# Kernel tuning notes

Measured on AMD Instinct MI355X. Metric: run time of the kernel, lower is better.

## Reference

```python
import jax, jax.numpy as jnp
import numpy as np


def setup_inputs() -> dict:
    key = jax.random.key(0)
    k1, k2, k3 = jax.random.split(key, 3)
    B, M, N, D = 8, 12, 32, 256
    C = N * N          # Conv2d channel dim == N*N (see permute/view in source)
    R = 2              # reduction
    x = jax.random.normal(k1, (B, M, N, D), dtype=jnp.float32)
    W1 = jax.random.normal(k2, (C // R, C), dtype=jnp.float32) * 0.02  # Conv2d(C, C//R, 1, bias=False)
    W2 = jax.random.normal(k3, (C, C // R), dtype=jnp.float32) * 0.02  # Conv2d(C//R, C, 1, bias=False)
    return {"x": x, "W1": W1, "W2": W2}


def _mycorr(x):
    # Pearson correlation across feature dim D -> [B, M, N, N] adjacency
    xm = x - x.mean(axis=-1, keepdims=True)
    cov = jnp.einsum('bmnd,bmkd->bmnk', xm, xm)
    diag = jnp.diagonal(cov, axis1=-2, axis2=-1)                 # [B, M, N]
    norm = jnp.sqrt(jnp.clip(diag, 1e-12))
    return cov / (norm[..., :, None] * norm[..., None, :])


def reference(x, W1, W2):
    B, M, N, D = x.shape
    adj = _mycorr(x)

    # Fused pairwise-combo + mean over concat dim (2D):
    #   cat([Wh_i, pos_ij * Wh_j], -1).mean(-1) = (sum_d Wh_i + sum_d pos_ij*Wh_j) / (2D)
    # pos_ij[d] = 1 where Wh_i[d] == Wh_j[d] else 2   (source's where(diff==0, 1, 2))
    Wi = x[:, :, :, None, :]          # [B, M, N, 1, D]
    Wj = x[:, :, None, :, :]          # [B, M, 1, N, D]
    pos = jnp.where(Wi == Wj, jnp.float32(1.0), jnp.float32(2.0))
    e0 = (x.sum(-1)[:, :, :, None] + (pos * Wj).sum(-1)) / (2.0 * D)  # [B, M, N, N]

    # squeeze-excite style 1x1-conv MLP over the N*N channel dim
    ef = e0.reshape(B, M, N * N).transpose(0, 2, 1)                   # [B, C=N*N, M]
    h = jax.nn.relu(jnp.einsum('oc,bcm->bom', W1, ef))                # [B, C//R, M]
    e2 = jnp.einsum('co,bom->bcm', W2, h)                             # [B, C, M]
    e = jax.nn.sigmoid(e2.transpose(0, 2, 1).reshape(B, M, N, N))

    att = jnp.where(adj > 0, e, jnp.float32(-1e12))
    att = jax.nn.softmax(att, axis=-1)
    return jnp.einsum('bmnk,bmkd->bmnd', att, x)
```

## Files before the change

### kernel.cpp

```cpp
#include <hip/hip_runtime.h>


__device__ __forceinline__ float sum4(float4 v){ return v.x+v.y+v.z+v.w; }
__device__ __forceinline__ float dot4(float4 a, float4 b){
    return a.x*b.x + a.y*b.y + a.z*b.z + a.w*b.w;
}
__device__ __forceinline__ void fma4s(float4& a, float s, float4 v){
    a.x += s*v.x; a.y += s*v.y; a.z += s*v.z; a.w += s*v.w;
}

__global__ __launch_bounds__(256) void k1(const float* __restrict__ x,
                                          const float* __restrict__ W1,
                                          float* __restrict__ A1t,
                                          float* __restrict__ Sg,
                                          float* __restrict__ covg) {
    int bid = blockIdx.x;
    if (bid < 128) {
        __shared__ float Rl[4][32];
        __shared__ float Cl[4][32];
        int w = threadIdx.x >> 6, l = threadIdx.x & 63;
        int o = bid*4 + w;
        const float4* W14 = (const float4*)(W1 + o*1024);
        float4 v0 = W14[l], v1 = W14[l+64], v2 = W14[l+128], v3 = W14[l+192];
        float r0 = sum4(v0), r1 = sum4(v1), r2 = sum4(v2), r3 = sum4(v3);
        #pragma unroll
        for (int m = 1; m < 8; m <<= 1) {
            r0 += __shfl_xor(r0, m, 8);
            r1 += __shfl_xor(r1, m, 8);
            r2 += __shfl_xor(r2, m, 8);
            r3 += __shfl_xor(r3, m, 8);
        }
        float4 cp;
        cp.x = v0.x+v1.x+v2.x+v3.x; cp.y = v0.y+v1.y+v2.y+v3.y;
        cp.z = v0.z+v1.z+v2.z+v3.z; cp.w = v0.w+v1.w+v2.w+v3.w;
        #pragma unroll
        for (int m = 8; m < 64; m <<= 1) {
            cp.x += __shfl_xor(cp.x, m);
            cp.y += __shfl_xor(cp.y, m);
            cp.z += __shfl_xor(cp.z, m);
            cp.w += __shfl_xor(cp.w, m);
        }
        if ((l & 7) == 0) {
            int nb = l >> 3;
            Rl[w][nb]    = r0; Rl[w][nb+8]  = r1;
            Rl[w][nb+16] = r2; Rl[w][nb+24] = r3;
        }
        if (l < 8) *((float4*)&Cl[w][l*4]) = cp;
        __syncthreads();
        if (l < 32) {
            float a = (Rl[w][l] + 2.f*Cl[w][l] - W1[o*1024 + 33*l]) * (1.f/512.f);
            A1t[l*512 + o] = a;
        }
    } else {
        int bm = bid - 128;
        int t = threadIdx.x;
        __shared__ float4 xs4[32][65];
        __shared__ float Gp[8][32][36];
        __shared__ alignas(16) float S_l[32];
        const float4* x4 = (const float4*)x;
        #pragma unroll
        for (int i = 0; i < 8; ++i) {
            int idx = t + 256*i;
            xs4[idx >> 6][idx & 63] = x4[bm*2048 + idx];
        }
        __syncthreads();
        {
            int n = t >> 3, dq = t & 7;
            float s = 0.f;
            #pragma unroll
            for (int j = 0; j < 8; ++j) s += sum4(xs4[n][dq + 8*j]);
            s += __shfl_xor(s, 1, 8);
            s += __shfl_xor(s, 2, 8);
            s += __shfl_xor(s, 4, 8);
            if (dq == 0) { S_l[n] = s; Sg[bm*32 + n] = s; }
        }
        {
            int qs = t >> 5, tid = t & 31, rt = tid >> 2, ct = tid & 3;
            float g[4][8];
            #pragma unroll
            for (int i = 0; i < 4; ++i)
                #pragma unroll
                for (int j = 0; j < 8; ++j) g[i][j] = 0.f;
            #pragma unroll
            for (int qq = 0; qq < 8; ++qq) {
                int q = qs*8 + qq;
                float4 a0 = xs4[rt][q],    a1 = xs4[rt+8][q];
                float4 a2 = xs4[rt+16][q], a3 = xs4[rt+24][q];
                #pragma unroll
                for (int j = 0; j < 8; ++j) {
                    float4 b = xs4[ct + 4*j][q];
                    g[0][j] += dot4(a0, b); g[1][j] += dot4(a1, b);
                    g[2][j] += dot4(a2, b); g[3][j] += dot4(a3, b);
                }
            }
            #pragma unroll
            for (int i = 0; i < 4; ++i)
                #pragma unroll
                for (int j = 0; j < 8; ++j)
                    Gp[qs][rt + 8*i][ct + 4*j] = g[i][j];
        }
        __syncthreads();
        {
            int n = t >> 3, k0 = (t & 7)*4;
            float4 g = {0.f,0.f,0.f,0.f};
            #pragma unroll
            for (int qs = 0; qs < 8; ++qs) {
                float4 p = *((const float4*)&Gp[qs][n][k0]);
                g.x += p.x; g.y += p.y; g.z += p.z; g.w += p.w;
            }
            float sn = S_l[n] * (1.f/256.f);
            float4 sk = *((const float4*)&S_l[k0]);
            float4 cv;
            cv.x = g.x - sn*sk.x; cv.y = g.y - sn*sk.y;
            cv.z = g.z - sn*sk.z; cv.w = g.w - sn*sk.w;
            ((float4*)covg)[bm*256 + t] = cv;
        }
    }
}

__global__ __launch_bounds__(256) void k2(const float* __restrict__ W2,
                                          const float* __restrict__ A1t,
                                          const float* __restrict__ Sg,
                                          float* __restrict__ Et) {
    __shared__ alignas(16) float S_l[8][32];
    __shared__ float hl[8][516];
    int t = threadIdx.x;
    int cT = blockIdx.x, bmG = blockIdx.y;
    {
        int bl = t >> 5, n = t & 31;
        S_l[bl][n] = Sg[(bmG*8 + bl)*32 + n];
    }
    __syncthreads();
    {
        const float4* A4 = (const float4*)A1t;
        #pragma unroll
        for (int part = 0; part < 4; ++part) {
            int o4 = part*256 + t;
            int bl = o4 >> 7, ol = o4 & 127;
            float4 hacc = {0.f,0.f,0.f,0.f};
            #pragma unroll 8
            for (int n = 0; n < 32; ++n)
                fma4s(hacc, S_l[bl][n], A4[n*128 + ol]);
            hacc.x = fmaxf(hacc.x, 0.f); hacc.y = fmaxf(hacc.y, 0.f);
            hacc.z = fmaxf(hacc.z, 0.f); hacc.w = fmaxf(hacc.w, 0.f);
            *((float4*)&hl[bl][ol*4]) = hacc;
        }
    }
    __syncthreads();
    {
        int olane = t & 15, cg = t >> 4;
        const float4* W24 = (const float4*)W2;
        #pragma unroll
        for (int ci = 0; ci < 4; ++ci) {
            int c = cT*64 + cg*4 + ci;
            float acc[8] = {0.f,0.f,0.f,0.f,0.f,0.f,0.f,0.f};
            #pragma unroll
            for (int oo = 0; oo < 8; ++oo) {
                float4 w = W24[c*128 + oo*16 + olane];
                #pragma unroll
                for (int bl = 0; bl < 8; ++bl)
                    acc[bl] += dot4(w, *((const float4*)&hl[bl][(oo*16+olane)*4]));
            }
            #pragma unroll
            for (int bl = 0; bl < 8; ++bl) {
                float a = acc[bl];
                a += __shfl_xor(a, 1, 16);
                a += __shfl_xor(a, 2, 16);
                a += __shfl_xor(a, 4, 16);
                a += __shfl_xor(a, 8, 16);
                if (olane == 0)
                    Et[(bmG*8 + bl)*1024 + c] = 1.f / (1.f + __expf(-a));
            }
        }
    }
}

__global__ __launch_bounds__(256) void k4(const float* __restrict__ x,
                                          const float* __restrict__ covg,
                                          const float* __restrict__ Et,
                                          float* __restrict__ out) {
    int bm = blockIdx.x >> 1;
    int h  = blockIdx.x & 1;
    int t  = threadIdx.x;
    __shared__ float4 xs4[32][33];
    __shared__ float att_l[32][36];
    const float4* x4 = (const float4*)x;
    #pragma unroll
    for (int i = 0; i < 4; ++i) {
        int idx = t + 256*i;
        int n = idx >> 5, dq = idx & 31;
        xs4[n][dq] = x4[bm*2048 + n*64 + h*32 + dq];
    }
    {
        float4 cv = ((const float4*)covg)[bm*256 + t];
        float4 e  = ((const float4*)Et)[bm*256 + t];
        float4 lg;
        lg.x = cv.x > 0.f ? e.x : -1e12f;
        lg.y = cv.y > 0.f ? e.y : -1e12f;
        lg.z = cv.z > 0.f ? e.z : -1e12f;
        lg.w = cv.w > 0.f ? e.w : -1e12f;
        float m = fmaxf(fmaxf(lg.x, lg.y), fmaxf(lg.z, lg.w));
        m = fmaxf(m, __shfl_xor(m, 1, 8));
        m = fmaxf(m, __shfl_xor(m, 2, 8));
        m = fmaxf(m, __shfl_xor(m, 4, 8));
        float4 p;
        p.x = __expf(lg.x - m); p.y = __expf(lg.y - m);
        p.z = __expf(lg.z - m); p.w = __expf(lg.w - m);
        float s = p.x + p.y + p.z + p.w;
        s += __shfl_xor(s, 1, 8);
        s += __shfl_xor(s, 2, 8);
        s += __shfl_xor(s, 4, 8);
        float inv = 1.f / s;
        p.x *= inv; p.y *= inv; p.z *= inv; p.w *= inv;
        *((float4*)&att_l[t >> 3][(t & 7)*4]) = p;
    }
    __syncthreads();
    {
        int txl = t & 31, wy = t >> 5;
        int r0 = wy*4;
        float4 acc0={0,0,0,0}, acc1={0,0,0,0}, acc2={0,0,0,0}, acc3={0,0,0,0};
        #pragma unroll
        for (int kq = 0; kq < 8; ++kq) {
            float4 xa = xs4[kq*4+0][txl];
            float4 xb = xs4[kq*4+1][txl];
            float4 xc = xs4[kq*4+2][txl];
            float4 xd = xs4[kq*4+3][txl];
            float4 w0 = *((const float4*)&att_l[r0+0][kq*4]);
            float4 w1 = *((const float4*)&att_l[r0+1][kq*4]);
            float4 w2 = *((const float4*)&att_l[r0+2][kq*4]);
            float4 w3 = *((const float4*)&att_l[r0+3][kq*4]);
            fma4s(acc0,w0.x,xa); fma4s(acc0,w0.y,xb); fma4s(acc0,w0.z,xc); fma4s(acc0,w0.w,xd);
            fma4s(acc1,w1.x,xa); fma4s(acc1,w1.y,xb); fma4s(acc1,w1.z,xc); fma4s(acc1,w1.w,xd);
            fma4s(acc2,w2.x,xa); fma4s(acc2,w2.y,xb); fma4s(acc2,w2.z,xc); fma4s(acc2,w2.w,xd);
            fma4s(acc3,w3.x,xa); fma4s(acc3,w3.y,xb); fma4s(acc3,w3.z,xc); fma4s(acc3,w3.w,xd);
        }
        float4* out4 = (float4*)out;
        out4[bm*2048 + (r0+0)*64 + h*32 + txl] = acc0;
        out4[bm*2048 + (r0+1)*64 + h*32 + txl] = acc1;
        out4[bm*2048 + (r0+2)*64 + h*32 + txl] = acc2;
        out4[bm*2048 + (r0+3)*64 + h*32 + txl] = acc3;
    }
}

extern "C" void kernel_launch(void* const* d_in, const int* in_sizes, int n_in,
                              void* d_out, int out_size, void* d_ws, size_t ws_size,
                              hipStream_t stream) {
    const float* x  = (const float*)d_in[0];
    const float* W1 = (const float*)d_in[1];
    const float* W2 = (const float*)d_in[2];
    float* out = (float*)d_out;
    float* ws  = (float*)d_ws;

    float* A1t  = ws;
    float* Sg   = ws + 16384;
    float* covg = ws + 19456;
    float* Et   = ws + 117760;

    k1<<<224, 256, 0, stream>>>(x, W1, A1t, Sg, covg);
    k2<<<dim3(16, 12), 256, 0, stream>>>(W2, A1t, Sg, Et);
    k4<<<192, 256, 0, stream>>>(x, covg, Et, out);
}
```

Measured before the change: 86.91 us.

## Fuse covariance, SE MLP and softmax-aggregate into one per-(b,m) kernel

Splits out the W1 precompute into its own small kernel. The covariance, hidden-layer MLP, W2 projection with sigmoid, masked softmax and attention aggregation now run in one kernel with one block per (b,m), using shared memory only. This removes two launches and the global round trips for the covariance, row sums and gate values. In exchange, each of the 96 blocks re-reads all of W2 with no batching across (b,m), so W2 traffic rises. Only 96 blocks run, which leaves many compute units idle.

```diff
diff --git a/kernel.cpp b/kernel.cpp
--- a/kernel.cpp
+++ b/kernel.cpp
@@ -9,191 +9,156 @@
     a.x += s*v.x; a.y += s*v.y; a.z += s*v.z; a.w += s*v.w;
 }
 
-__global__ __launch_bounds__(256) void k1(const float* __restrict__ x,
-                                          const float* __restrict__ W1,
-                                          float* __restrict__ A1t,
-                                          float* __restrict__ Sg,
-                                          float* __restrict__ covg) {
-    int bid = blockIdx.x;
-    if (bid < 128) {
-        __shared__ float Rl[4][32];
-        __shared__ float Cl[4][32];
-        int w = threadIdx.x >> 6, l = threadIdx.x & 63;
-        int o = bid*4 + w;
-        const float4* W14 = (const float4*)(W1 + o*1024);
-        float4 v0 = W14[l], v1 = W14[l+64], v2 = W14[l+128], v3 = W14[l+192];
-        float r0 = sum4(v0), r1 = sum4(v1), r2 = sum4(v2), r3 = sum4(v3);
-        #pragma unroll
-        for (int m = 1; m < 8; m <<= 1) {
-            r0 += __shfl_xor(r0, m, 8);
-            r1 += __shfl_xor(r1, m, 8);
-            r2 += __shfl_xor(r2, m, 8);
-            r3 += __shfl_xor(r3, m, 8);
-        }
-        float4 cp;
-        cp.x = v0.x+v1.x+v2.x+v3.x; cp.y = v0.y+v1.y+v2.y+v3.y;
-        cp.z = v0.z+v1.z+v2.z+v3.z; cp.w = v0.w+v1.w+v2.w+v3.w;
-        #pragma unroll
-        for (int m = 8; m < 64; m <<= 1) {
-            cp.x += __shfl_xor(cp.x, m);
-            cp.y += __shfl_xor(cp.y, m);
-            cp.z += __shfl_xor(cp.z, m);
-            cp.w += __shfl_xor(cp.w, m);
-        }
-        if ((l & 7) == 0) {
-            int nb = l >> 3;
-            Rl[w][nb]    = r0; Rl[w][nb+8]  = r1;
-            Rl[w][nb+16] = r2; Rl[w][nb+24] = r3;
-        }
-        if (l < 8) *((float4*)&Cl[w][l*4]) = cp;
-        __syncthreads();
-        if (l < 32) {
-            float a = (Rl[w][l] + 2.f*Cl[w][l] - W1[o*1024 + 33*l]) * (1.f/512.f);
-            A1t[l*512 + o] = a;
-        }
-    } else {
-        int bm = bid - 128;
-        int t = threadIdx.x;
-        __shared__ float4 xs4[32][65];
-        __shared__ float Gp[8][32][36];
-        __shared__ alignas(16) float S_l[32];
-        const float4* x4 = (const float4*)x;
-        #pragma unroll
-        for (int i = 0; i < 8; ++i) {
-            int idx = t + 256*i;
-            xs4[idx >> 6][idx & 63] = x4[bm*2048 + idx];
-        }
-        __syncthreads();
-        {
-            int n = t >> 3, dq = t & 7;
-            float s = 0.f;
-            #pragma unroll
-            for (int j = 0; j < 8; ++j) s += sum4(xs4[n][dq + 8*j]);
-            s += __shfl_xor(s, 1, 8);
-            s += __shfl_xor(s, 2, 8);
-            s += __shfl_xor(s, 4, 8);
-            if (dq == 0) { S_l[n] = s; Sg[bm*32 + n] = s; }
-        }
-        {
-            int qs = t >> 5, tid = t & 31, rt = tid >> 2, ct = tid & 3;
-            float g[4][8];
-            #pragma unroll
-            for (int i = 0; i < 4; ++i)
-                #pragma unroll
-                for (int j = 0; j < 8; ++j) g[i][j] = 0.f;
-            #pragma unroll
-            for (int qq = 0; qq < 8; ++qq) {
-                int q = qs*8 + qq;
-                float4 a0 = xs4[rt][q],    a1 = xs4[rt+8][q];
-                float4 a2 = xs4[rt+16][q], a3 = xs4[rt+24][q];
-                #pragma unroll
-                for (int j = 0; j < 8; ++j) {
-                    float4 b = xs4[ct + 4*j][q];
-                    g[0][j] += dot4(a0, b); g[1][j] += dot4(a1, b);
-                    g[2][j] += dot4(a2, b); g[3][j] += dot4(a3, b);
-                }
+__global__ __launch_bounds__(256) void kA(const float* __restrict__ W1,
+                                          float* __restrict__ A1t) {
+    __shared__ float Rl[4][32];
+    __shared__ float Cl[4][32];
+    int w = threadIdx.x >> 6, l = threadIdx.x & 63;
+    int o = blockIdx.x*4 + w;
+    const float4* W14 = (const float4*)(W1 + o*1024);
+    float4 v0 = W14[l], v1 = W14[l+64], v2 = W14[l+128], v3 = W14[l+192];
+    float r0 = sum4(v0), r1 = sum4(v1), r2 = sum4(v2), r3 = sum4(v3);
+    #pragma unroll
+    for (int m = 1; m < 8; m <<= 1) {
+        r0 += __shfl_xor(r0, m, 8);
+        r1 += __shfl_xor(r1, m, 8);
+        r2 += __shfl_xor(r2, m, 8);
+        r3 += __shfl_xor(r3, m, 8);
+    }
+    float4 cp;
+    cp.x = v0.x+v1.x+v2.x+v3.x; cp.y = v0.y+v1.y+v2.y+v3.y;
+    cp.z = v0.z+v1.z+v2.z+v3.z; cp.w = v0.w+v1.w+v2.w+v3.w;
+    #pragma unroll
+    for (int m = 8; m < 64; m <<= 1) {
+        cp.x += __shfl_xor(cp.x, m);
+        cp.y += __shfl_xor(cp.y, m);
+        cp.z += __shfl_xor(cp.z, m);
+        cp.w += __shfl_xor(cp.w, m);
+    }
+    if ((l & 7) == 0) {
+        int nb = l >> 3;
+        Rl[w][nb]    = r0; Rl[w][nb+8]  = r1;
+        Rl[w][nb+16] = r2; Rl[w][nb+24] = r3;
+    }
+    if (l < 8) *((float4*)&Cl[w][l*4]) = cp;
+    __syncthreads();
+    if (l < 32) {
+        float a = (Rl[w][l] + 2.f*Cl[w][l] - W1[o*1024 + 33*l]) * (1.f/512.f);
+        A1t[l*512 + o] = a;
+    }
+}
+
+__global__ __launch_bounds__(256) void kM(const float* __restrict__ x,
+                                          const float* __restrict__ A1t,
+                                          const float* __restrict__ W2,
+                                          float* __restrict__ out) {
+    int bm = blockIdx.x;
+    int t  = threadIdx.x;
+    __shared__ float4 xs4[32][65];
+    __shared__ float Gp[4][32][37];
+    __shared__ alignas(16) float S_l[32];
+    __shared__ alignas(16) float hl[520];
+    __shared__ alignas(16) float el[1024];
+    __shared__ alignas(16) float att_l[32][36];
+
+    const float4* x4 = (const float4*)x;
+    #pragma unroll
+    for (int i = 0; i < 8; ++i) {
+        int idx = t + 256*i;
+        xs4[idx >> 6][idx & 63] = x4[bm*2048 + idx];
+    }
+    __syncthreads();
+
+    {
+        int n = t >> 3, dq = t & 7;
+        float s = 0.f;
+        #pragma unroll
+        for (int j = 0; j < 8; ++j) s += sum4(xs4[n][dq + 8*j]);
+        s += __shfl_xor(s, 1, 8);
+        s += __shfl_xor(s, 2, 8);
+        s += __shfl_xor(s, 4, 8);
+        if (dq == 0) S_l[n] = s;
+    }
+    {
+        int w = t >> 6, l = t & 63, rt = l >> 3, ct = l & 7;
+        float g[4][4];
+        #pragma unroll
+        for (int i = 0; i < 4; ++i)
+            #pragma unroll
+            for (int j = 0; j < 4; ++j) g[i][j] = 0.f;
+        #pragma unroll 4
+        for (int qq = 0; qq < 16; ++qq) {
+            int q = w*16 + qq;
+            float4 a0 = xs4[rt][q],    a1 = xs4[rt+8][q];
+            float4 a2 = xs4[rt+16][q], a3 = xs4[rt+24][q];
+            #pragma unroll
+            for (int j = 0; j < 4; ++j) {
+                float4 b = xs4[ct + 8*j][q];
+                g[0][j] += dot4(a0, b); g[1][j] += dot4(a1, b);
+                g[2][j] += dot4(a2, b); g[3][j] += dot4(a3, b);
             }
-            #pragma unroll
-            for (int i = 0; i < 4; ++i)
-                #pragma unroll
-                for (int j = 0; j < 8; ++j)
-                    Gp[qs][rt + 8*i][ct + 4*j] = g[i][j];
-        }
-        __syncthreads();
-        {
-            int n = t >> 3, k0 = (t & 7)*4;
-            float4 g = {0.f,0.f,0.f,0.f};
-            #pragma unroll
-            for (int qs = 0; qs < 8; ++qs) {
-                float4 p = *((const float4*)&Gp[qs][n][k0]);
-                g.x += p.x; g.y += p.y; g.z += p.z; g.w += p.w;
-            }
-            float sn = S_l[n] * (1.f/256.f);
-            float4 sk = *((const float4*)&S_l[k0]);
-            float4 cv;
-            cv.x = g.x - sn*sk.x; cv.y = g.y - sn*sk.y;
-            cv.z = g.z - sn*sk.z; cv.w = g.w - sn*sk.w;
-            ((float4*)covg)[bm*256 + t] = cv;
-        }
-    }
-}
-
-__global__ __launch_bounds__(256) void k2(const float* __restrict__ W2,
-                                          const float* __restrict__ A1t,
-                                          const float* __restrict__ Sg,
-                                          float* __restrict__ Et) {
-    __shared__ alignas(16) float S_l[8][32];
-    __shared__ float hl[8][516];
-    int t = threadIdx.x;
-    int cT = blockIdx.x, bmG = blockIdx.y;
-    {
-        int bl = t >> 5, n = t & 31;
-        S_l[bl][n] = Sg[(bmG*8 + bl)*32 + n];
-    }
-    __syncthreads();
-    {
+        }
+        #pragma unroll
+        for (int i = 0; i < 4; ++i)
+            #pragma unroll
+            for (int j = 0; j < 4; ++j)
+                Gp[w][rt + 8*i][ct + 8*j] = g[i][j];
+    }
+    __syncthreads();
+
+    {
+        int n = t >> 3, k0 = (t & 7)*4;
+        float sn = S_l[n] * (1.f/256.f);
+        float4 cv;
+        #pragma unroll
+        for (int c = 0; c < 4; ++c) {
+            float g = Gp[0][n][k0+c] + Gp[1][n][k0+c]
+                    + Gp[2][n][k0+c] + Gp[3][n][k0+c];
+            float v = g - sn * S_l[k0+c];
+            if (c == 0) cv.x = v; else if (c == 1) cv.y = v;
+            else if (c == 2) cv.z = v; else cv.w = v;
+        }
+        *((float4*)&att_l[n][k0]) = cv;
+    }
+    if (t >= 128) {
+        int o4 = t - 128;
         const float4* A4 = (const float4*)A1t;
-        #pragma unroll
-        for (int part = 0; part < 4; ++part) {
-            int o4 = part*256 + t;
-            int bl = o4 >> 7, ol = o4 & 127;
-            float4 hacc = {0.f,0.f,0.f,0.f};
-            #pragma unroll 8
-            for (int n = 0; n < 32; ++n)
-                fma4s(hacc, S_l[bl][n], A4[n*128 + ol]);
-            hacc.x = fmaxf(hacc.x, 0.f); hacc.y = fmaxf(hacc.y, 0.f);
-            hacc.z = fmaxf(hacc.z, 0.f); hacc.w = fmaxf(hacc.w, 0.f);
-            *((float4*)&hl[bl][ol*4]) = hacc;
-        }
-    }
-    __syncthreads();
+        float4 hacc = {0.f,0.f,0.f,0.f};
+        #pragma unroll 8
+        for (int n = 0; n < 32; ++n)
+            fma4s(hacc, S_l[n], A4[n*128 + o4]);
+        hacc.x = fmaxf(hacc.x, 0.f); hacc.y = fmaxf(hacc.y, 0.f);
+        hacc.z = fmaxf(hacc.z, 0.f); hacc.w = fmaxf(hacc.w, 0.f);
+        *((float4*)&hl[o4*4]) = hacc;
+    }
+    __syncthreads();
+
     {
         int olane = t & 15, cg = t >> 4;
         const float4* W24 = (const float4*)W2;
-        #pragma unroll
-        for (int ci = 0; ci < 4; ++ci) {
-            int c = cT*64 + cg*4 + ci;
-            float acc[8] = {0.f,0.f,0.f,0.f,0.f,0.f,0.f,0.f};
+        for (int ci = 0; ci < 64; ++ci) {
+            int c = cg*64 + ((ci + cg) & 63);
+            float acc = 0.f;
             #pragma unroll
             for (int oo = 0; oo < 8; ++oo) {
                 float4 w = W24[c*128 + oo*16 + olane];
-                #pragma unroll
-                for (int bl = 0; bl < 8; ++bl)
-                    acc[bl] += dot4(w, *((const float4*)&hl[bl][(oo*16+olane)*4]));
+                float4 h = *((const float4*)&hl[(oo*16 + olane)*4]);
+                acc += dot4(w, h);
             }
-            #pragma unroll
-            for (int bl = 0; bl < 8; ++bl) {
-                float a = acc[bl];
-                a += __shfl_xor(a, 1, 16);
-                a += __shfl_xor(a, 2, 16);
-                a += __shfl_xor(a, 4, 16);
-                a += __shfl_xor(a, 8, 16);
-                if (olane == 0)
-                    Et[(bmG*8 + bl)*1024 + c] = 1.f / (1.f + __expf(-a));
-            }
-        }
-    }
-}
-
-__global__ __launch_bounds__(256) void k4(const float* __restrict__ x,
-                                          const float* __restrict__ covg,
-                                          const float* __restrict__ Et,
-                                          float* __restrict__ out) {
-    int bm = blockIdx.x >> 1;
-    int h  = blockIdx.x & 1;
-    int t  = threadIdx.x;
-    __shared__ float4 xs4[32][33];
-    __shared__ float att_l[32][36];
-    const float4* x4 = (const float4*)x;
-    #pragma unroll
-    for (int i = 0; i < 4; ++i) {
-        int idx = t + 256*i;
-        int n = idx >> 5, dq = idx & 31;
-        xs4[n][dq] = x4[bm*2048 + n*64 + h*32 + dq];
-    }
-    {
-        float4 cv = ((const float4*)covg)[bm*256 + t];
-        float4 e  = ((const float4*)Et)[bm*256 + t];
+            acc += __shfl_xor(acc, 1, 16);
+            acc += __shfl_xor(acc, 2, 16);
+            acc += __shfl_xor(acc, 4, 16);
+            acc += __shfl_xor(acc, 8, 16);
+            if (olane == 0)
+                el[c] = 1.f / (1.f + __expf(-acc));
+        }
+    }
+    __syncthreads();
+
+    {
+        int r = t >> 3, q = t & 7;
+        float4 cv = *((const float4*)&att_l[r][q*4]);
+        float4 e  = ((const float4*)el)[t];
         float4 lg;
         lg.x = cv.x > 0.f ? e.x : -1e12f;
         lg.y = cv.y > 0.f ? e.y : -1e12f;
@@ -212,33 +177,37 @@
         s += __shfl_xor(s, 4, 8);
         float inv = 1.f / s;
         p.x *= inv; p.y *= inv; p.z *= inv; p.w *= inv;
-        *((float4*)&att_l[t >> 3][(t & 7)*4]) = p;
-    }
-    __syncthreads();
-    {
-        int txl = t & 31, wy = t >> 5;
-        int r0 = wy*4;
-        float4 acc0={0,0,0,0}, acc1={0,0,0,0}, acc2={0,0,0,0}, acc3={0,0,0,0};
-        #pragma unroll
-        for (int kq = 0; kq < 8; ++kq) {
-            float4 xa = xs4[kq*4+0][txl];
-            float4 xb = xs4[kq*4+1][txl];
-            float4 xc = xs4[kq*4+2][txl];
-            float4 xd = xs4[kq*4+3][txl];
-            float4 w0 = *((const float4*)&att_l[r0+0][kq*4]);
-            float4 w1 = *((const float4*)&att_l[r0+1][kq*4]);
-            float4 w2 = *((const float4*)&att_l[r0+2][kq*4]);
-            float4 w3 = *((const float4*)&att_l[r0+3][kq*4]);
-            fma4s(acc0,w0.x,xa); fma4s(acc0,w0.y,xb); fma4s(acc0,w0.z,xc); fma4s(acc0,w0.w,xd);
-            fma4s(acc1,w1.x,xa); fma4s(acc1,w1.y,xb); fma4s(acc1,w1.z,xc); fma4s(acc1,w1.w,xd);
-            fma4s(acc2,w2.x,xa); fma4s(acc2,w2.y,xb); fma4s(acc2,w2.z,xc); fma4s(acc2,w2.w,xd);
-            fma4s(acc3,w3.x,xa); fma4s(acc3,w3.y,xb); fma4s(acc3,w3.z,xc); fma4s(acc3,w3.w,xd);
-        }
+        *((float4*)&att_l[r][q*4]) = p;
+    }
+    __syncthreads();
+
+    {
+        int tx = t & 63, wy = t >> 6;
         float4* out4 = (float4*)out;
-        out4[bm*2048 + (r0+0)*64 + h*32 + txl] = acc0;
-        out4[bm*2048 + (r0+1)*64 + h*32 + txl] = acc1;
-        out4[bm*2048 + (r0+2)*64 + h*32 + txl] = acc2;
-        out4[bm*2048 + (r0+3)*64 + h*32 + txl] = acc3;
+        #pragma unroll
+        for (int g = 0; g < 2; ++g) {
+            int r0 = wy*8 + g*4;
+            float4 acc0={0,0,0,0}, acc1={0,0,0,0}, acc2={0,0,0,0}, acc3={0,0,0,0};
+            #pragma unroll
+            for (int kq = 0; kq < 8; ++kq) {
+                float4 xa = xs4[kq*4+0][tx];
+                float4 xb = xs4[kq*4+1][tx];
+                float4 xc = xs4[kq*4+2][tx];
+                float4 xd = xs4[kq*4+3][tx];
+                float4 w0 = *((const float4*)&att_l[r0+0][kq*4]);
+                float4 w1 = *((const float4*)&att_l[r0+1][kq*4]);
+                float4 w2 = *((const float4*)&att_l[r0+2][kq*4]);
+                float4 w3 = *((const float4*)&att_l[r0+3][kq*4]);
+                fma4s(acc0,w0.x,xa); fma4s(acc0,w0.y,xb); fma4s(acc0,w0.z,xc); fma4s(acc0,w0.w,xd);
+                fma4s(acc1,w1.x,xa); fma4s(acc1,w1.y,xb); fma4s(acc1,w1.z,xc); fma4s(acc1,w1.w,xd);
+                fma4s(acc2,w2.x,xa); fma4s(acc2,w2.y,xb); fma4s(acc2,w2.z,xc); fma4s(acc2,w2.w,xd);
+                fma4s(acc3,w3.x,xa); fma4s(acc3,w3.y,xb); fma4s(acc3,w3.z,xc); fma4s(acc3,w3.w,xd);
+            }
+            out4[bm*2048 + (r0+0)*64 + tx] = acc0;
+            out4[bm*2048 + (r0+1)*64 + tx] = acc1;
+            out4[bm*2048 + (r0+2)*64 + tx] = acc2;
+            out4[bm*2048 + (r0+3)*64 + tx] = acc3;
+        }
     }
 }
 
@@ -249,14 +218,8 @@
     const float* W1 = (const float*)d_in[1];
     const float* W2 = (const float*)d_in[2];
     float* out = (float*)d_out;
-    float* ws  = (float*)d_ws;
-
-    float* A1t  = ws;
-    float* Sg   = ws + 16384;
-    float* covg = ws + 19456;
-    float* Et   = ws + 117760;
-
-    k1<<<224, 256, 0, stream>>>(x, W1, A1t, Sg, covg);
-    k2<<<dim3(16, 12), 256, 0, stream>>>(W2, A1t, Sg, Et);
-    k4<<<192, 256, 0, stream>>>(x, covg, Et, out);
-}
+    float* A1t = (float*)d_ws;
+
+    kA<<<128, 256, 0, stream>>>(W1, A1t);
+    kM<<<96, 256, 0, stream>>>(x, A1t, W2, out);
+}
```

After: 105.8 us. 1.22x slower.

## Split W1 prep into own kernel and fuse hidden-layer compute into covariance kernel

Applied to the files above, without the earlier changes.

The merged W1-reduction/covariance kernel is split in two. The covariance kernel now also computes the ReLU hidden activations per (b,m) from the row sums, and the W2 kernel just loads them instead of recomputing them from A1t for every column tile. The Gram tiling also changes from 8 to 4 partial slices, with more work per warp. This removes redundant hidden-layer work across the 16 column-tile blocks but adds a fourth launch and serialises the W1 prep before the covariance kernel.

```diff
diff --git a/kernel.cpp b/kernel.cpp
--- a/kernel.cpp
+++ b/kernel.cpp
@@ -9,142 +9,136 @@
     a.x += s*v.x; a.y += s*v.y; a.z += s*v.z; a.w += s*v.w;
 }
 
-__global__ __launch_bounds__(256) void k1(const float* __restrict__ x,
-                                          const float* __restrict__ W1,
-                                          float* __restrict__ A1t,
-                                          float* __restrict__ Sg,
-                                          float* __restrict__ covg) {
-    int bid = blockIdx.x;
-    if (bid < 128) {
-        __shared__ float Rl[4][32];
-        __shared__ float Cl[4][32];
-        int w = threadIdx.x >> 6, l = threadIdx.x & 63;
-        int o = bid*4 + w;
-        const float4* W14 = (const float4*)(W1 + o*1024);
-        float4 v0 = W14[l], v1 = W14[l+64], v2 = W14[l+128], v3 = W14[l+192];
-        float r0 = sum4(v0), r1 = sum4(v1), r2 = sum4(v2), r3 = sum4(v3);
-        #pragma unroll
-        for (int m = 1; m < 8; m <<= 1) {
-            r0 += __shfl_xor(r0, m, 8);
-            r1 += __shfl_xor(r1, m, 8);
-            r2 += __shfl_xor(r2, m, 8);
-            r3 += __shfl_xor(r3, m, 8);
-        }
-        float4 cp;
-        cp.x = v0.x+v1.x+v2.x+v3.x; cp.y = v0.y+v1.y+v2.y+v3.y;
-        cp.z = v0.z+v1.z+v2.z+v3.z; cp.w = v0.w+v1.w+v2.w+v3.w;
-        #pragma unroll
-        for (int m = 8; m < 64; m <<= 1) {
-            cp.x += __shfl_xor(cp.x, m);
-            cp.y += __shfl_xor(cp.y, m);
-            cp.z += __shfl_xor(cp.z, m);
-            cp.w += __shfl_xor(cp.w, m);
-        }
-        if ((l & 7) == 0) {
-            int nb = l >> 3;
-            Rl[w][nb]    = r0; Rl[w][nb+8]  = r1;
-            Rl[w][nb+16] = r2; Rl[w][nb+24] = r3;
-        }
-        if (l < 8) *((float4*)&Cl[w][l*4]) = cp;
-        __syncthreads();
-        if (l < 32) {
-            float a = (Rl[w][l] + 2.f*Cl[w][l] - W1[o*1024 + 33*l]) * (1.f/512.f);
-            A1t[l*512 + o] = a;
-        }
-    } else {
-        int bm = bid - 128;
-        int t = threadIdx.x;
-        __shared__ float4 xs4[32][65];
-        __shared__ float Gp[8][32][36];
-        __shared__ alignas(16) float S_l[32];
-        const float4* x4 = (const float4*)x;
-        #pragma unroll
-        for (int i = 0; i < 8; ++i) {
-            int idx = t + 256*i;
-            xs4[idx >> 6][idx & 63] = x4[bm*2048 + idx];
-        }
-        __syncthreads();
-        {
-            int n = t >> 3, dq = t & 7;
-            float s = 0.f;
-            #pragma unroll
-            for (int j = 0; j < 8; ++j) s += sum4(xs4[n][dq + 8*j]);
-            s += __shfl_xor(s, 1, 8);
-            s += __shfl_xor(s, 2, 8);
-            s += __shfl_xor(s, 4, 8);
-            if (dq == 0) { S_l[n] = s; Sg[bm*32 + n] = s; }
-        }
-        {
-            int qs = t >> 5, tid = t & 31, rt = tid >> 2, ct = tid & 3;
-            float g[4][8];
-            #pragma unroll
-            for (int i = 0; i < 4; ++i)
-                #pragma unroll
-                for (int j = 0; j < 8; ++j) g[i][j] = 0.f;
-            #pragma unroll
-            for (int qq = 0; qq < 8; ++qq) {
-                int q = qs*8 + qq;
-                float4 a0 = xs4[rt][q],    a1 = xs4[rt+8][q];
-                float4 a2 = xs4[rt+16][q], a3 = xs4[rt+24][q];
-                #pragma unroll
-                for (int j = 0; j < 8; ++j) {
-                    float4 b = xs4[ct + 4*j][q];
-                    g[0][j] += dot4(a0, b); g[1][j] += dot4(a1, b);
-                    g[2][j] += dot4(a2, b); g[3][j] += dot4(a3, b);
-                }
+__global__ __launch_bounds__(256) void kA(const float* __restrict__ W1,
+                                          float* __restrict__ A1t) {
+    __shared__ float Rl[4][32];
+    __shared__ float Cl[4][32];
+    int w = threadIdx.x >> 6, l = threadIdx.x & 63;
+    int o = blockIdx.x*4 + w;
+    const float4* W14 = (const float4*)(W1 + o*1024);
+    float4 v0 = W14[l], v1 = W14[l+64], v2 = W14[l+128], v3 = W14[l+192];
+    float r0 = sum4(v0), r1 = sum4(v1), r2 = sum4(v2), r3 = sum4(v3);
+    #pragma unroll
+    for (int m = 1; m < 8; m <<= 1) {
+        r0 += __shfl_xor(r0, m, 8);
+        r1 += __shfl_xor(r1, m, 8);
+        r2 += __shfl_xor(r2, m, 8);
+        r3 += __shfl_xor(r3, m, 8);
+    }
+    float4 cp;
+    cp.x = v0.x+v1.x+v2.x+v3.x; cp.y = v0.y+v1.y+v2.y+v3.y;
+    cp.z = v0.z+v1.z+v2.z+v3.z; cp.w = v0.w+v1.w+v2.w+v3.w;
+    #pragma unroll
+    for (int m = 8; m < 64; m <<= 1) {
+        cp.x += __shfl_xor(cp.x, m);
+        cp.y += __shfl_xor(cp.y, m);
+        cp.z += __shfl_xor(cp.z, m);
+        cp.w += __shfl_xor(cp.w, m);
+    }
+    if ((l & 7) == 0) {
+        int nb = l >> 3;
+        Rl[w][nb]    = r0; Rl[w][nb+8]  = r1;
+        Rl[w][nb+16] = r2; Rl[w][nb+24] = r3;
+    }
+    if (l < 8) *((float4*)&Cl[w][l*4]) = cp;
+    __syncthreads();
+    if (l < 32) {
+        float a = (Rl[w][l] + 2.f*Cl[w][l] - W1[o*1024 + 33*l]) * (1.f/512.f);
+        A1t[l*512 + o] = a;
+    }
+}
+
+__global__ __launch_bounds__(256) void kC(const float* __restrict__ x,
+                                          const float* __restrict__ A1t,
+                                          float* __restrict__ covg,
+                                          float* __restrict__ Ht) {
+    int bm = blockIdx.x;
+    int t  = threadIdx.x;
+    __shared__ float4 xs4[32][65];
+    __shared__ float Gp[4][32][37];
+    __shared__ alignas(16) float S_l[32];
+
+    const float4* x4 = (const float4*)x;
+    #pragma unroll
+    for (int i = 0; i < 8; ++i) {
+        int idx = t + 256*i;
+        xs4[idx >> 6][idx & 63] = x4[bm*2048 + idx];
+    }
+    __syncthreads();
+    {
+        int n = t >> 3, dq = t & 7;
+        float s = 0.f;
+        #pragma unroll
+        for (int j = 0; j < 8; ++j) s += sum4(xs4[n][dq + 8*j]);
+        s += __shfl_xor(s, 1, 8);
+        s += __shfl_xor(s, 2, 8);
+        s += __shfl_xor(s, 4, 8);
+        if (dq == 0) S_l[n] = s;
+    }
+    {
+        int w = t >> 6, l = t & 63, rt = l >> 3, ct = l & 7;
+        float g[4][4];
+        #pragma unroll
+        for (int i = 0; i < 4; ++i)
+            #pragma unroll
+            for (int j = 0; j < 4; ++j) g[i][j] = 0.f;
+        #pragma unroll 4
+        for (int qq = 0; qq < 16; ++qq) {
+            int q = w*16 + qq;
+            float4 a0 = xs4[rt][q],    a1 = xs4[rt+8][q];
+            float4 a2 = xs4[rt+16][q], a3 = xs4[rt+24][q];
+            #pragma unroll
+            for (int j = 0; j < 4; ++j) {
+                float4 b = xs4[ct + 8*j][q];
+                g[0][j] += dot4(a0, b); g[1][j] += dot4(a1, b);
+                g[2][j] += dot4(a2, b); g[3][j] += dot4(a3, b);
             }
-            #pragma unroll
-            for (int i = 0; i < 4; ++i)
-                #pragma unroll
-                for (int j = 0; j < 8; ++j)
-                    Gp[qs][rt + 8*i][ct + 4*j] = g[i][j];
-        }
-        __syncthreads();
-        {
-            int n = t >> 3, k0 = (t & 7)*4;
-            float4 g = {0.f,0.f,0.f,0.f};
-            #pragma unroll
-            for (int qs = 0; qs < 8; ++qs) {
-                float4 p = *((const float4*)&Gp[qs][n][k0]);
-                g.x += p.x; g.y += p.y; g.z += p.z; g.w += p.w;
-            }
-            float sn = S_l[n] * (1.f/256.f);
-            float4 sk = *((const float4*)&S_l[k0]);
-            float4 cv;
-            cv.x = g.x - sn*sk.x; cv.y = g.y - sn*sk.y;
-            cv.z = g.z - sn*sk.z; cv.w = g.w - sn*sk.w;
-            ((float4*)covg)[bm*256 + t] = cv;
-        }
-    }
-}
-
-__global__ __launch_bounds__(256) void k2(const float* __restrict__ W2,
-                                          const float* __restrict__ A1t,
-                                          const float* __restrict__ Sg,
+        }
+        #pragma unroll
+        for (int i = 0; i < 4; ++i)
+            #pragma unroll
+            for (int j = 0; j < 4; ++j)
+                Gp[w][rt + 8*i][ct + 8*j] = g[i][j];
+    }
+    __syncthreads();
+    {
+        int n = t >> 3, k0 = (t & 7)*4;
+        float sn = S_l[n] * (1.f/256.f);
+        float4 cv;
+        #pragma unroll
+        for (int c = 0; c < 4; ++c) {
+            float g = Gp[0][n][k0+c] + Gp[1][n][k0+c]
+                    + Gp[2][n][k0+c] + Gp[3][n][k0+c];
+            float v = g - sn * S_l[k0+c];
+            if (c == 0) cv.x = v; else if (c == 1) cv.y = v;
+            else if (c == 2) cv.z = v; else cv.w = v;
+        }
+        ((float4*)covg)[bm*256 + t] = cv;
+    }
+    if (t < 128) {
+        const float4* A4 = (const float4*)A1t;
+        float4 hacc = {0.f,0.f,0.f,0.f};
+        #pragma unroll 8
+        for (int n = 0; n < 32; ++n)
+            fma4s(hacc, S_l[n], A4[n*128 + t]);
+        hacc.x = fmaxf(hacc.x, 0.f); hacc.y = fmaxf(hacc.y, 0.f);
+        hacc.z = fmaxf(hacc.z, 0.f); hacc.w = fmaxf(hacc.w, 0.f);
+        ((float4*)Ht)[bm*128 + t] = hacc;
+    }
+}
+
+__global__ __launch_bounds__(256) void kE(const float* __restrict__ W2,
+                                          const float* __restrict__ Ht,
                                           float* __restrict__ Et) {
-    __shared__ alignas(16) float S_l[8][32];
     __shared__ float hl[8][516];
     int t = threadIdx.x;
     int cT = blockIdx.x, bmG = blockIdx.y;
-    {
-        int bl = t >> 5, n = t & 31;
-        S_l[bl][n] = Sg[(bmG*8 + bl)*32 + n];
-    }
-    __syncthreads();
-    {
-        const float4* A4 = (const float4*)A1t;
-        #pragma unroll
-        for (int part = 0; part < 4; ++part) {
-            int o4 = part*256 + t;
-            int bl = o4 >> 7, ol = o4 & 127;
-            float4 hacc = {0.f,0.f,0.f,0.f};
-            #pragma unroll 8
-            for (int n = 0; n < 32; ++n)
-                fma4s(hacc, S_l[bl][n], A4[n*128 + ol]);
-            hacc.x = fmaxf(hacc.x, 0.f); hacc.y = fmaxf(hacc.y, 0.f);
-            hacc.z = fmaxf(hacc.z, 0.f); hacc.w = fmaxf(hacc.w, 0.f);
-            *((float4*)&hl[bl][ol*4]) = hacc;
-        }
+    const float4* Ht4 = (const float4*)Ht;
+    #pragma unroll
+    for (int i = 0; i < 4; ++i) {
+        int idx = t + 256*i;
+        int bl = idx >> 7, o4 = idx & 127;
+        *((float4*)&hl[bl][o4*4]) = Ht4[(bmG*8 + bl)*128 + o4];
     }
     __syncthreads();
     {
@@ -175,7 +169,7 @@
     }
 }
 
-__global__ __launch_bounds__(256) void k4(const float* __restrict__ x,
+__global__ __launch_bounds__(256) void kO(const float* __restrict__ x,
                                           const float* __restrict__ covg,
                                           const float* __restrict__ Et,
                                           float* __restrict__ out) {
@@ -252,11 +246,12 @@
     float* ws  = (float*)d_ws;
 
     float* A1t  = ws;
-    float* Sg   = ws + 16384;
-    float* covg = ws + 19456;
-    float* Et   = ws + 117760;
-
-    k1<<<224, 256, 0, stream>>>(x, W1, A1t, Sg, covg);
-    k2<<<dim3(16, 12), 256, 0, stream>>>(W2, A1t, Sg, Et);
-    k4<<<192, 256, 0, stream>>>(x, covg, Et, out);
-}
+    float* covg = ws + 16384;
+    float* Ht   = ws + 114688;
+    float* Et   = ws + 163840;
+
+    kA<<<128, 256, 0, stream>>>(W1, A1t);
+    kC<<<96, 256, 0, stream>>>(x, A1t, covg, Ht);
+    kE<<<dim3(16, 12), 256, 0, stream>>>(W2, Ht, Et);
+    kO<<<192, 256, 0, stream>>>(x, covg, Et, out);
+}
```

New measurement: 83.99 us. -3.4%, faster.
